# Kernel tuning notes

Hardware: AMD Instinct MI355X
Metric: run time of the kernel (lower is better)

Reference implementation:

```python
import jax, jax.numpy as jnp
import numpy as np

EPS = 1e-5


def reference(hidden_states, mu_x, W_x1, W_x2, x_bias, W_r, W_k, W_v, W_g,
              A_w, B_w, b_w, bonus, gn_weight, gn_bias, W_o):
    B, T, D = hidden_states.shape
    Hh = bonus.shape[0]
    x = hidden_states
    # token shift: delta = shifted(x) - x, shifted pads one zero row at t=0
    shifted = jnp.pad(x, ((0, 0), (1, 0), (0, 0)))[:, :T]
    delta = shifted - x
    # x_proj: LerpLinear(D -> 5*lr) -> tanh -> einsum with second weight viewed [D,5,lr]
    lr = W_x1.shape[0] // 5
    z = jnp.tanh((x + delta * mu_x) @ W_x1.T).reshape(B, T, 5, lr)
    mus = jnp.einsum('blnr,dnr->blnd', z, W_x2.reshape(D, 5, lr)) + x_bias  # [B,T,5,D]
    r_mu, w_mu, k_mu, v_mu, g_mu = (mus[:, :, i] for i in range(5))
    # DDLerpLinear projections: linear(x + delta * mu)
    r = (x + delta * r_mu) @ W_r.T                                 # [B,T,KD]
    w = jnp.tanh((x + delta * w_mu) @ A_w.T) @ B_w.T + b_w          # LoRA w/ tanh
    k = (x + delta * k_mu) @ W_k.T
    v = (x + delta * v_mu) @ W_v.T                                 # [B,T,VD]
    g = (x + delta * g_mu) @ W_g.T
    K = W_r.shape[0] // Hh
    V = W_v.shape[0] // Hh
    r = r.reshape(B, T, Hh, K)
    k = k.reshape(B, T, Hh, K)
    w = -jnp.exp(w.reshape(B, T, Hh, K))  # log-decay, in (-inf, 0)
    v = v.reshape(B, T, Hh, V)
    u = bonus                              # [Hh, K]

    def step(S, inp):
        q_t, k_t, v_t, w_t = inp           # [B,Hh,K],[B,Hh,K],[B,Hh,V],[B,Hh,K]
        kv = k_t[..., :, None] * v_t[..., None, :]                  # [B,Hh,K,V]
        o_t = jnp.einsum('bhk,bhkv->bhv', q_t, S + u[None, :, :, None] * kv)
        S = jnp.exp(w_t)[..., None] * S + kv
        return S, o_t

    S0 = jnp.zeros((B, Hh, K, V), dtype=x.dtype)
    xs = (jnp.swapaxes(r, 0, 1), jnp.swapaxes(k, 0, 1),
          jnp.swapaxes(v, 0, 1), jnp.swapaxes(w, 0, 1))
    _, o = jax.lax.scan(step, S0, xs)       # o: [T,B,Hh,V]
    o = jnp.swapaxes(o, 0, 1)               # [B,T,Hh,V]
    # GroupNorm(num_heads, value_dim): normalize each head's V channels per token
    mean = o.mean(-1, keepdims=True)
    var = o.var(-1, keepdims=True)
    o = (o - mean) / jnp.sqrt(var + EPS)
    o = o.reshape(B, T, Hh * V) * gn_weight + gn_bias
    o = o * jax.nn.silu(g)                  # swish gate
    return o @ W_o.T


def setup_inputs() -> dict:
    key = jax.random.key(0)
    ks = jax.random.split(key, 16)
    B, T, D = 8, 2048, 1024
    Hh, KD, VD, LR, GLR = 4, 512, 1024, 32, 64
    s = 0.02
    w = lambda k, shape: jax.random.normal(k, shape, jnp.float32) * s
    return {
        'hidden_states': jax.random.normal(ks[0], (B, T, D), jnp.float32),
        'mu_x': w(ks[1], (D,)),
        'W_x1': w(ks[2], (5 * LR, D)),
        'W_x2': w(ks[3], (D, 5 * LR)),
        'x_bias': jnp.zeros((5, D), jnp.float32),
        'W_r': w(ks[4], (KD, D)),
        'W_k': w(ks[5], (KD, D)),
        'W_v': w(ks[6], (VD, D)),
        'W_g': w(ks[7], (VD, D)),
        'A_w': w(ks[8], (GLR, D)),
        'B_w': w(ks[9], (KD, GLR)),
        'b_w': jnp.zeros((KD,), jnp.float32),
        'bonus': w(ks[10], (Hh, KD // Hh)),
        'gn_weight': jnp.ones((VD,), jnp.float32),
        'gn_bias': jnp.zeros((VD,), jnp.float32),
        'W_o': w(ks[11], (D, VD)),
    }
```

## Files before the change

### kernel.cpp

```cpp
#include <hip/hip_runtime.h>
#include <hip/hip_bf16.h>
#include <hip/hip_fp16.h>
#include <cstdint>


typedef _Float16 half8 __attribute__((ext_vector_type(8)));
typedef float f32x4 __attribute__((ext_vector_type(4)));
typedef unsigned short ushort8 __attribute__((ext_vector_type(8)));

#define CL 512
#define NP (CL / 2)

__device__ __forceinline__ float hbits2f(unsigned short us) {
    __half h; *reinterpret_cast<unsigned short*>(&h) = us; return __half2float(h);
}
__device__ __forceinline__ unsigned short f2h(float f) {
    __half h = __float2half(f);
    return *reinterpret_cast<unsigned short*>(&h);
}
__device__ __forceinline__ float2 up2(unsigned int u) {
    return make_float2(hbits2f((unsigned short)(u & 0xFFFF)),
                       hbits2f((unsigned short)(u >> 16)));
}

__global__ void cast16(const float* __restrict__ src, __half* __restrict__ dst, int n4)
{
    const int i = blockIdx.x * blockDim.x + threadIdx.x;
    if (i >= n4) return;
    const float4 f = *(const float4*)(src + (size_t)i * 4);
    ushort4 u;
    u.x = f2h(f.x); u.y = f2h(f.y); u.z = f2h(f.z); u.w = f2h(f.w);
    *(ushort4*)(dst + (size_t)i * 4) = u;
}

__global__ void k_xw_h(const float* __restrict__ X, const float* __restrict__ mu,
                       __half* __restrict__ XW, int M, int T)
{
    const size_t i4 = (size_t)blockIdx.x * blockDim.x + threadIdx.x;
    if (i4 >= (size_t)M * 256) return;
    const size_t idx = i4 * 4;
    const int m = (int)(idx >> 10);
    const int d = (int)(idx & 1023);
    const int t = m & (T - 1);
    const float4 xv = *(const float4*)(X + idx);
    const float4 m4 = *(const float4*)(mu + d);
    float4 xp = make_float4(0.f, 0.f, 0.f, 0.f);
    if (t > 0) xp = *(const float4*)(X + idx - 1024);
    ushort4 o;
    o.x = f2h(xv.x + (xp.x - xv.x) * m4.x);
    o.y = f2h(xv.y + (xp.y - xv.y) * m4.y);
    o.z = f2h(xv.z + (xp.z - xv.z) * m4.z);
    o.w = f2h(xv.w + (xp.w - xv.w) * m4.w);
    *(ushort4*)(XW + idx) = o;
}

#define TS 40

__global__ __launch_bounds__(256) void gemm16(
    const __half* __restrict__ A, int lda,
    const __half* __restrict__ B, int ldb,
    void* __restrict__ Cv, int ldc,
    int M, int N, int K,
    const float* __restrict__ bias, int epi,
    const float* __restrict__ X, int T)
{
    __shared__ __align__(16) _Float16 As[128 * TS];
    __shared__ __align__(16) _Float16 Bs[128 * TS];

    const int tid = threadIdx.x;

    const int nwg = gridDim.x * gridDim.y;
    int p = blockIdx.y * gridDim.x + blockIdx.x;
    if (!(nwg & 7)) p = (p & 7) * (nwg >> 3) + (p >> 3);
    const int bx = p % gridDim.x, by = p / gridDim.x;

    const int m0 = by * 128;
    const int n0 = bx * 128;
    const int wave = tid >> 6, lane = tid & 63;
    const int wm = wave >> 1, wn = wave & 1;
    const int lr = lane & 15, lk = lane >> 4;

    const int srow = tid >> 1;
    const int sseg = (tid & 1) * 16;

    f32x4 acc[4][4] = {};

    for (int k0 = 0; k0 < K; k0 += 32) {
        const __half* ap = A + (size_t)(m0 + srow) * lda + k0 + sseg;
        ushort8 a0 = *(const ushort8*)ap;
        ushort8 a1 = *(const ushort8*)(ap + 8);
        ushort8 b0 = {0,0,0,0,0,0,0,0}, b1 = {0,0,0,0,0,0,0,0};
        if (n0 + srow < N) {
            const __half* bp = B + (size_t)(n0 + srow) * ldb + k0 + sseg;
            b0 = *(const ushort8*)bp;
            b1 = *(const ushort8*)(bp + 8);
        }
        __syncthreads();
        *(ushort8*)&As[srow * TS + sseg + 0] = a0;
        *(ushort8*)&As[srow * TS + sseg + 8] = a1;
        *(ushort8*)&Bs[srow * TS + sseg + 0] = b0;
        *(ushort8*)&Bs[srow * TS + sseg + 8] = b1;
        __syncthreads();

        half8 af[4], bf[4];
#pragma unroll
        for (int f = 0; f < 4; f++) {
            af[f] = *(const half8*)&As[(wm * 64 + f * 16 + lr) * TS + lk * 8];
            bf[f] = *(const half8*)&Bs[(wn * 64 + f * 16 + lr) * TS + lk * 8];
        }
#pragma unroll
        for (int fm = 0; fm < 4; fm++)
#pragma unroll
            for (int fn = 0; fn < 4; fn++)
                acc[fm][fn] = __builtin_amdgcn_mfma_f32_16x16x32_f16(
                    af[fm], bf[fn], acc[fm][fn], 0, 0, 0);
    }

#pragma unroll
    for (int fm = 0; fm < 4; fm++) {
#pragma unroll
        for (int fn = 0; fn < 4; fn++) {
#pragma unroll
            for (int j = 0; j < 4; j++) {
                const int gm = m0 + wm * 64 + fm * 16 + lk * 4 + j;
                const int gn = n0 + wn * 64 + fn * 16 + lr;
                if (gn >= N) continue;
                float a = acc[fm][fn][j];
                if (epi == 1) {
                    a = tanhf(a);
                    ((__half*)Cv)[(size_t)gm * ldc + gn] = __float2half(a);
                } else if (epi == 2) {
                    a += bias[gn];
                    const float xv = X[(size_t)gm * 1024 + gn];
                    float xp = 0.f;
                    if (gm & (T - 1)) xp = X[(size_t)(gm - 1) * 1024 + gn];
                    ((__half*)Cv)[(size_t)gm * ldc + gn] =
                        __float2half(xv + (xp - xv) * a);
                } else if (epi == 3) {
                    a += bias[gn];
                    ((__half*)Cv)[(size_t)gm * ldc + gn] = __float2half(a);
                } else if (epi == 4) {
                    ((float*)Cv)[(size_t)gm * ldc + gn] = a;
                } else {
                    ((__half*)Cv)[(size_t)gm * ldc + gn] = __float2half(a);
                }
            }
        }
    }
}

__global__ __launch_bounds__(256) void k_prep(
    const __half* __restrict__ R, const __half* __restrict__ Kk,
    const __half* __restrict__ W, const float* __restrict__ bonus,
    unsigned* __restrict__ Eu, float* __restrict__ RU, int T)
{
    const int tok = blockIdx.x;
    const int b = tok >> 11, t = tok & 2047;
    const int h = threadIdx.x >> 6, lane = threadIdx.x & 63;
    const size_t base = (size_t)tok * 512 + h * 128 + 2 * lane;
    const unsigned rr = *(const unsigned*)(R + base);
    const unsigned kk = *(const unsigned*)(Kk + base);
    const unsigned ww = *(const unsigned*)(W + base);
    const float2 rf = up2(rr), kf = up2(kk), wf = up2(ww);
    const float d0 = __expf(-__expf(wf.x));
    const float d1 = __expf(-__expf(wf.y));
    const float2 uf = *(const float2*)(bonus + h * 128 + 2 * lane);
    float ru = rf.x * uf.x * kf.x + rf.y * uf.y * kf.y;
#pragma unroll
    for (int off = 1; off < 64; off <<= 1) ru += __shfl_xor(ru, off);
    const int bh = b * 4 + h;
    unsigned* ep = Eu + (size_t)(bh * T + t) * 192;
    uint2 rkw;
    rkw.x = (rr & 0xFFFFu) | (kk << 16);
    rkw.y = (rr >> 16) | (kk & 0xFFFF0000u);
    *(uint2*)(ep + 2 * lane) = rkw;
    ep[128 + lane] = (unsigned)f2h(d0) | ((unsigned)f2h(d1) << 16);
    if (lane == 0) RU[(size_t)bh * T + t] = ru;
}

template<bool PART>
__global__ __launch_bounds__(256) void rwkv_coop(
    const uint4* __restrict__ E, const __half* __restrict__ V,
    const float* __restrict__ RU, const float* __restrict__ Cin,
    float* __restrict__ Cout, float* __restrict__ Abuf,
    __half* __restrict__ O, int T)
{
    __shared__ uint4 sE[4][96];
    __shared__ uint4 sV[4][16];
    __shared__ float sRU[4][2];

    const int p = blockIdx.x;
    int bh, c, vq;
    if (PART) {
        const int l = (p & 7) * 48 + (p >> 3);
        bh = l / 12; const int rem = l - bh * 12; c = rem >> 2; vq = rem & 3;
    } else {
        const int l = (p & 7) * 64 + (p >> 3);
        bh = l >> 4; c = (l >> 2) & 3; vq = l & 3;
    }
    const int b = bh >> 2, h = bh & 3;
    const int tid = threadIdx.x;
    const int w = tid >> 6, lane = tid & 63;
    const int kg = tid & 15, vg = tid >> 4;
    const int t0 = c * CL;

    const uint4* Eg = E + (size_t)(bh * T + t0) * 48;
    const uint4* Vgp = (const uint4*)(V + ((size_t)b * T + t0) * 1024 + h * 256 + vq * 64);
    const float* RUp = RU + (size_t)bh * T + t0;
    __half* Op = O + ((size_t)b * T + t0) * 1024 + h * 256 + vq * 64 + vg * 4;

    float S[32];
    float Aacc[8];
    if (!PART && c) {
        const float* Sp = Cin + ((size_t)(c - 1) * 32 + bh) * 32768 + vq * 64 + vg * 4;
#pragma unroll
        for (int kk = 0; kk < 8; kk++) {
            const float4 s4 = *(const float4*)(Sp + (size_t)(kg * 8 + kk) * 256);
            S[kk * 4 + 0] = s4.x; S[kk * 4 + 1] = s4.y;
            S[kk * 4 + 2] = s4.z; S[kk * 4 + 3] = s4.w;
        }
    } else {
#pragma unroll
        for (int j = 0; j < 32; j++) S[j] = 0.f;
    }
#pragma unroll
    for (int j = 0; j < 8; j++) Aacc[j] = 1.f;

    const int i0 = (kg * 2) ^ ((kg * 2) >> 3);
    const int i1 = (kg * 2 + 1) ^ ((kg * 2 + 1) >> 3);

#define ISSUE(BE, BV, BR, PP)                                                 \
    if (w < 2 && (PP) < NP) {                                                 \
        const int tt = (PP) * 2 + w;                                          \
        if (lane < 48)      BE = Eg[(size_t)tt * 48 + lane];                  \
        else if (lane < 56) BV = Vgp[(size_t)tt * 128 + (lane - 48)];         \
        if (lane == 56)     BR = RUp[tt];                                     \
    }

#define STAGE(BE, BV, BR, SLOT)                                               \
    if (w < 2) {                                                              \
        if (lane < 32)      sE[SLOT][w * 48 + (lane ^ (lane >> 3))] = BE;     \
        else if (lane < 48) sE[SLOT][w * 48 + lane] = BE;                     \
        else if (lane < 56) sV[SLOT][w * 8 + (lane - 48)] = BV;               \
        if (lane == 56)     sRU[SLOT][w] = BR;                                \
    }

#define BAR() do {                                                            \
        asm volatile("s_waitcnt lgkmcnt(0)" ::: "memory");                    \
        __builtin_amdgcn_s_barrier();                                         \
        __builtin_amdgcn_sched_barrier(0);                                    \
    } while (0)

#define COMPUTE(SLOT, SUB, TT)                                                \
    {                                                                         \
        const uint4 rka = sE[SLOT][(SUB) * 48 + i0];                          \
        const uint4 rkb = sE[SLOT][(SUB) * 48 + i1];                          \
        const uint4 dq  = sE[SLOT][(SUB) * 48 + 32 + kg];                     \
        const uint2 vw  = *(const uint2*)((const unsigned*)&sV[SLOT][(SUB) * 8] + vg * 2); \
        const unsigned rw_[8] = {rka.x, rka.y, rka.z, rka.w,                  \
                                 rkb.x, rkb.y, rkb.z, rkb.w};                 \
        const unsigned dw_[4] = {dq.x, dq.y, dq.z, dq.w};                     \
        float r_[8], k_[8], d_[8], vv_[4];                                    \
        _Pragma("unroll") for (int j = 0; j < 8; j++) {                       \
            const float2 rk = up2(rw_[j]); r_[j] = rk.x; k_[j] = rk.y;        \
        }                                                                     \
        _Pragma("unroll") for (int j = 0; j < 4; j++) {                       \
            const float2 dd = up2(dw_[j]); d_[2 * j] = dd.x; d_[2 * j + 1] = dd.y; \
        }                                                                     \
        { const float2 va = up2(vw.x), vb = up2(vw.y);                        \
          vv_[0] = va.x; vv_[1] = va.y; vv_[2] = vb.x; vv_[3] = vb.y; }       \
        float osum[4] = {0.f, 0.f, 0.f, 0.f};                                 \
        _Pragma("unroll") for (int kk = 0; kk < 8; kk++) {                    \
            _Pragma("unroll") for (int vi = 0; vi < 4; vi++) {                \
                osum[vi] = fmaf(r_[kk], S[kk * 4 + vi], osum[vi]);            \
                S[kk * 4 + vi] = fmaf(d_[kk], S[kk * 4 + vi], k_[kk] * vv_[vi]); \
            }                                                                 \
            if (PART) Aacc[kk] *= d_[kk];                                     \
        }                                                                     \
        if (!PART) {                                                          \
            _Pragma("unroll") for (int vi = 0; vi < 4; vi++) {                \
                osum[vi] += __shfl_xor(osum[vi], 1);                          \
                osum[vi] += __shfl_xor(osum[vi], 2);                          \
                osum[vi] += __shfl_xor(osum[vi], 4);                          \
                osum[vi] += __shfl_xor(osum[vi], 8);                          \
            }                                                                 \
            if (kg == 0) {                                                    \
                const float ru_ = sRU[SLOT][SUB];                             \
                ushort4 ou;                                                   \
                ou.x = f2h(osum[0] + ru_ * vv_[0]);                           \
                ou.y = f2h(osum[1] + ru_ * vv_[1]);                           \
                ou.z = f2h(osum[2] + ru_ * vv_[2]);                           \
                ou.w = f2h(osum[3] + ru_ * vv_[3]);                           \
                *(ushort4*)(Op + (size_t)(TT) * 1024) = ou;                   \
            }                                                                 \
        }                                                                     \
    }

#define COMPUTE2(SLOT, PP)  COMPUTE(SLOT, 0, (PP) * 2) COMPUTE(SLOT, 1, (PP) * 2 + 1)

    uint4 e0 = {}, e1 = {}, e2 = {}, e3 = {};
    uint4 v0 = {}, v1 = {}, v2 = {}, v3 = {};
    float r0 = 0.f, r1 = 0.f, r2 = 0.f, r3 = 0.f;

    ISSUE(e0, v0, r0, 0)
    ISSUE(e1, v1, r1, 1)
    ISSUE(e2, v2, r2, 2)
    ISSUE(e3, v3, r3, 3)
    STAGE(e0, v0, r0, 0)
    BAR();

    for (int ps = 0; ps < NP; ps += 4) {
        STAGE(e1, v1, r1, 1)
        ISSUE(e0, v0, r0, ps + 4)
        COMPUTE2(0, ps)
        BAR();
        STAGE(e2, v2, r2, 2)
        ISSUE(e1, v1, r1, ps + 5)
        COMPUTE2(1, ps + 1)
        BAR();
        STAGE(e3, v3, r3, 3)
        ISSUE(e2, v2, r2, ps + 6)
        COMPUTE2(2, ps + 2)
        BAR();
        if (ps + 4 < NP) STAGE(e0, v0, r0, 0)
        ISSUE(e3, v3, r3, ps + 7)
        COMPUTE2(3, ps + 3)
        BAR();
    }

    if (PART) {
        float* Cw = Cout + ((size_t)c * 32 + bh) * 32768 + vq * 64 + vg * 4;
#pragma unroll
        for (int kk = 0; kk < 8; kk++) {
            float4 s4;
            s4.x = S[kk * 4 + 0]; s4.y = S[kk * 4 + 1];
            s4.z = S[kk * 4 + 2]; s4.w = S[kk * 4 + 3];
            *(float4*)(Cw + (size_t)(kg * 8 + kk) * 256) = s4;
        }
        if (vg == 0) {
            float* Aw = Abuf + ((size_t)c * 32 + bh) * 128 + kg * 8;
#pragma unroll
            for (int kk = 0; kk < 8; kk++) Aw[kk] = Aacc[kk];
        }
    }
#undef ISSUE
#undef STAGE
#undef BAR
#undef COMPUTE
#undef COMPUTE2
}

__global__ __launch_bounds__(256) void rwkv_comb(
    float* __restrict__ C, const float* __restrict__ A)
{
    const int gid = blockIdx.x * 256 + threadIdx.x;
    const int bh = gid >> 15;
    const int elem = gid & 32767;
    const int k = elem >> 8;
    float s = C[(size_t)bh * 32768 + elem];
    s = A[(size_t)(32 + bh) * 128 + k] * s +
        C[((size_t)32 + bh) * 32768 + elem];
    C[((size_t)32 + bh) * 32768 + elem] = s;
    s = A[(size_t)(64 + bh) * 128 + k] * s +
        C[((size_t)64 + bh) * 32768 + elem];
    C[((size_t)64 + bh) * 32768 + elem] = s;
}

__global__ __launch_bounds__(256) void gn_gate(
    const __half* __restrict__ Obuf, const __half* __restrict__ G,
    const float* __restrict__ gnw, const float* __restrict__ gnb,
    __half* __restrict__ Y)
{
    const int token = blockIdx.x;
    const int wave = threadIdx.x >> 6, lane = threadIdx.x & 63;
    const size_t base = (size_t)token * 1024 + wave * 256 + lane * 4;
    const ushort4 xu = *(const ushort4*)(Obuf + base);
    const float x0 = hbits2f(xu.x), x1 = hbits2f(xu.y),
                x2 = hbits2f(xu.z), x3 = hbits2f(xu.w);
    float sum = x0 + x1 + x2 + x3;
    float ssq = x0 * x0 + x1 * x1 + x2 * x2 + x3 * x3;
#pragma unroll
    for (int off = 32; off >= 1; off >>= 1) {
        sum += __shfl_xor(sum, off);
        ssq += __shfl_xor(ssq, off);
    }
    const float mean = sum * (1.f / 256.f);
    const float var = ssq * (1.f / 256.f) - mean * mean;
    const float rstd = rsqrtf(var + 1e-5f);
    const int c0 = wave * 256 + lane * 4;
    const float4 w4 = *(const float4*)(gnw + c0);
    const float4 b4 = *(const float4*)(gnb + c0);
    const ushort4 gu = *(const ushort4*)(G + base);
    const float g0 = hbits2f(gu.x), g1 = hbits2f(gu.y),
                g2 = hbits2f(gu.z), g3 = hbits2f(gu.w);
    ushort4 y;
    y.x = f2h(((x0 - mean) * rstd * w4.x + b4.x) * (g0 / (1.f + __expf(-g0))));
    y.y = f2h(((x1 - mean) * rstd * w4.y + b4.y) * (g1 / (1.f + __expf(-g1))));
    y.z = f2h(((x2 - mean) * rstd * w4.z + b4.z) * (g2 / (1.f + __expf(-g2))));
    y.w = f2h(((x3 - mean) * rstd * w4.w + b4.w) * (g3 / (1.f + __expf(-g3))));
    *(ushort4*)(Y + base) = y;
}

extern "C" void kernel_launch(void* const* d_in, const int* in_sizes, int n_in,
                              void* d_out, int out_size, void* d_ws, size_t ws_size,
                              hipStream_t stream)
{
    (void)in_sizes; (void)n_in; (void)out_size; (void)ws_size;
    const float* x      = (const float*)d_in[0];
    const float* mu_x   = (const float*)d_in[1];
    const float* W_x1   = (const float*)d_in[2];
    const float* W_x2   = (const float*)d_in[3];
    const float* x_bias = (const float*)d_in[4];
    const float* W_r    = (const float*)d_in[5];
    const float* W_k    = (const float*)d_in[6];
    const float* W_v    = (const float*)d_in[7];
    const float* W_g    = (const float*)d_in[8];
    const float* A_w    = (const float*)d_in[9];
    const float* B_w    = (const float*)d_in[10];
    const float* b_w    = (const float*)d_in[11];
    const float* bonus  = (const float*)d_in[12];
    const float* gnw    = (const float*)d_in[13];
    const float* gnb    = (const float*)d_in[14];
    const float* W_o    = (const float*)d_in[15];

    const int B = 8, T = 2048, M = B * T;

    __half* xwh  = (__half*)d_out;
    __half* inbh = xwh + (size_t)M * 1024;

    __half* z   = (__half*)d_ws;
    __half* w1  = z   + (size_t)M * 160;
    __half* rs  = w1  + (size_t)M * 64;
    __half* ks  = rs  + (size_t)M * 512;
    __half* wsm = ks  + (size_t)M * 512;
    __half* vs  = wsm + (size_t)M * 512;
    __half* gs  = vs  + (size_t)M * 1024;
    float*  ru  = (float*)(gs + (size_t)M * 1024);
    __half* wgt = (__half*)(ru + (size_t)32 * T);
    __half* oh  = rs;
    __half* yb  = wsm;
    float*  Cbuf = (float*)wsm;
    float*  Abuf = (float*)z;

    __half* W_x1h = wgt;
    __half* W_x2h = W_x1h + 163840;
    __half* W_rh  = W_x2h + 163840;
    __half* W_kh  = W_rh + 524288;
    __half* W_vh  = W_kh + 524288;
    __half* W_gh  = W_vh + 1048576;
    __half* A_wh  = W_gh + 1048576;
    __half* B_wh  = A_wh + 65536;
    __half* W_oh  = B_wh + 32768;

    const dim3 blk(256);
    auto cgrid = [](int n) { return dim3((n / 4 + 255) / 256); };
    cast16<<<cgrid(163840), blk, 0, stream>>>(W_x1, W_x1h, 163840 / 4);
    cast16<<<cgrid(163840), blk, 0, stream>>>(W_x2, W_x2h, 163840 / 4);
    cast16<<<cgrid(524288), blk, 0, stream>>>(W_r, W_rh, 524288 / 4);
    cast16<<<cgrid(524288), blk, 0, stream>>>(W_k, W_kh, 524288 / 4);
    cast16<<<cgrid(1048576), blk, 0, stream>>>(W_v, W_vh, 1048576 / 4);
    cast16<<<cgrid(1048576), blk, 0, stream>>>(W_g, W_gh, 1048576 / 4);
    cast16<<<cgrid(65536), blk, 0, stream>>>(A_w, A_wh, 65536 / 4);
    cast16<<<cgrid(32768), blk, 0, stream>>>(B_w, B_wh, 32768 / 4);
    cast16<<<cgrid(1048576), blk, 0, stream>>>(W_o, W_oh, 1048576 / 4);

    k_xw_h<<<(M * 256 + 255) / 256, blk, 0, stream>>>(x, mu_x, xwh, M, T);

    auto ggrid = [&](int N) { return dim3((N + 127) / 128, M / 128); };

    gemm16<<<ggrid(160), blk, 0, stream>>>(xwh, 1024, W_x1h, 1024, z, 160,
                                           M, 160, 1024, nullptr, 1, nullptr, T);

    for (int n = 0; n < 5; ++n) {
        gemm16<<<ggrid(1024), blk, 0, stream>>>(z + n * 32, 160, W_x2h + n * 32, 160,
                                                inbh, 1024, M, 1024, 32,
                                                x_bias + n * 1024, 2, x, T);
        if (n == 1) {
            gemm16<<<ggrid(64), blk, 0, stream>>>(inbh, 1024, A_wh, 1024, w1, 64,
                                                  M, 64, 1024, nullptr, 1, nullptr, T);
            gemm16<<<ggrid(512), blk, 0, stream>>>(w1, 64, B_wh, 64, wsm, 512,
                                                   M, 512, 64, b_w, 3, nullptr, T);
        } else {
            __half* Cp = (n == 0) ? rs : (n == 2) ? ks : (n == 3) ? vs : gs;
            const __half* Wp = (n == 0) ? W_rh : (n == 2) ? W_kh : (n == 3) ? W_vh : W_gh;
            const int N = (n == 0 || n == 2) ? 512 : 1024;
            gemm16<<<ggrid(N), blk, 0, stream>>>(inbh, 1024, Wp, 1024, Cp, N,
                                                 M, N, 1024, nullptr, 0, nullptr, T);
        }
    }

    k_prep<<<dim3(M), blk, 0, stream>>>(rs, ks, wsm, bonus,
                                        (unsigned*)d_out, ru, T);

    rwkv_coop<true><<<dim3(384), blk, 0, stream>>>(
        (const uint4*)d_out, vs, ru, Cbuf, Cbuf, Abuf, oh, T);
    rwkv_comb<<<dim3(4096), blk, 0, stream>>>(Cbuf, Abuf);
    rwkv_coop<false><<<dim3(512), blk, 0, stream>>>(
        (const uint4*)d_out, vs, ru, Cbuf, Cbuf, Abuf, oh, T);

    gn_gate<<<dim3(M), blk, 0, stream>>>(oh, gs, gnw, gnb, yb);

    gemm16<<<ggrid(1024), blk, 0, stream>>>(yb, 1024, W_oh, 1024, d_out, 1024,
                                            M, 1024, 1024, nullptr, 4, nullptr, T);
}
```

Before: 1.222 ms.

## Load GEMM tiles directly to LDS, halve scan chunk length, store carry states in fp16

```diff
diff --git a/kernel.cpp b/kernel.cpp
--- a/kernel.cpp
+++ b/kernel.cpp
@@ -6,10 +6,10 @@
 
 typedef _Float16 half8 __attribute__((ext_vector_type(8)));
 typedef float f32x4 __attribute__((ext_vector_type(4)));
-typedef unsigned short ushort8 __attribute__((ext_vector_type(8)));
-
-#define CL 512
+
+#define CL 256
 #define NP (CL / 2)
+#define NC 8
 
 __device__ __forceinline__ float hbits2f(unsigned short us) {
     __half h; *reinterpret_cast<unsigned short*>(&h) = us; return __half2float(h);
@@ -21,6 +21,11 @@
 __device__ __forceinline__ float2 up2(unsigned int u) {
     return make_float2(hbits2f((unsigned short)(u & 0xFFFF)),
                        hbits2f((unsigned short)(u >> 16)));
+}
+__device__ __forceinline__ void gload_lds16(const void* g, void* l) {
+    __builtin_amdgcn_global_load_lds(
+        (const __attribute__((address_space(1))) unsigned*)g,
+        (__attribute__((address_space(3))) unsigned*)l, 16, 0, 0);
 }
 
 __global__ void cast16(const float* __restrict__ src, __half* __restrict__ dst, int n4)
@@ -54,8 +59,6 @@
     *(ushort4*)(XW + idx) = o;
 }
 
-#define TS 40
-
 __global__ __launch_bounds__(256) void gemm16(
     const __half* __restrict__ A, int lda,
     const __half* __restrict__ B, int ldb,
@@ -64,8 +67,8 @@
     const float* __restrict__ bias, int epi,
     const float* __restrict__ X, int T)
 {
-    __shared__ __align__(16) _Float16 As[128 * TS];
-    __shared__ __align__(16) _Float16 Bs[128 * TS];
+    __shared__ __align__(16) _Float16 As[128 * 32];
+    __shared__ __align__(16) _Float16 Bs[128 * 32];
 
     const int tid = threadIdx.x;
 
@@ -80,33 +83,33 @@
     const int wm = wave >> 1, wn = wave & 1;
     const int lr = lane & 15, lk = lane >> 4;
 
-    const int srow = tid >> 1;
-    const int sseg = (tid & 1) * 16;
+    const int srow = tid >> 2;
+    const int scol = (tid & 3) * 8;
+    const int arow0 = m0 + srow, arow1 = m0 + 64 + srow;
+    int brow0 = n0 + srow;      if (brow0 >= N) brow0 = N - 1;
+    int brow1 = n0 + 64 + srow; if (brow1 >= N) brow1 = N - 1;
+    char* dA = (char*)As + tid * 16;
+    char* dB = (char*)Bs + tid * 16;
 
     f32x4 acc[4][4] = {};
 
     for (int k0 = 0; k0 < K; k0 += 32) {
-        const __half* ap = A + (size_t)(m0 + srow) * lda + k0 + sseg;
-        ushort8 a0 = *(const ushort8*)ap;
-        ushort8 a1 = *(const ushort8*)(ap + 8);
-        ushort8 b0 = {0,0,0,0,0,0,0,0}, b1 = {0,0,0,0,0,0,0,0};
-        if (n0 + srow < N) {
-            const __half* bp = B + (size_t)(n0 + srow) * ldb + k0 + sseg;
-            b0 = *(const ushort8*)bp;
-            b1 = *(const ushort8*)(bp + 8);
-        }
+        const __half* gA0 = A + (size_t)arow0 * lda + k0 + scol;
+        const __half* gA1 = A + (size_t)arow1 * lda + k0 + scol;
+        const __half* gB0 = B + (size_t)brow0 * ldb + k0 + scol;
+        const __half* gB1 = B + (size_t)brow1 * ldb + k0 + scol;
         __syncthreads();
-        *(ushort8*)&As[srow * TS + sseg + 0] = a0;
-        *(ushort8*)&As[srow * TS + sseg + 8] = a1;
-        *(ushort8*)&Bs[srow * TS + sseg + 0] = b0;
-        *(ushort8*)&Bs[srow * TS + sseg + 8] = b1;
+        gload_lds16(gA0, dA);
+        gload_lds16(gA1, dA + 4096);
+        gload_lds16(gB0, dB);
+        gload_lds16(gB1, dB + 4096);
         __syncthreads();
 
         half8 af[4], bf[4];
 #pragma unroll
         for (int f = 0; f < 4; f++) {
-            af[f] = *(const half8*)&As[(wm * 64 + f * 16 + lr) * TS + lk * 8];
-            bf[f] = *(const half8*)&Bs[(wn * 64 + f * 16 + lr) * TS + lk * 8];
+            af[f] = *(const half8*)&As[(wm * 64 + f * 16 + lr) * 32 + lk * 8];
+            bf[f] = *(const half8*)&Bs[(wn * 64 + f * 16 + lr) * 32 + lk * 8];
         }
 #pragma unroll
         for (int fm = 0; fm < 4; fm++)
@@ -181,8 +184,8 @@
 template<bool PART>
 __global__ __launch_bounds__(256) void rwkv_coop(
     const uint4* __restrict__ E, const __half* __restrict__ V,
-    const float* __restrict__ RU, const float* __restrict__ Cin,
-    float* __restrict__ Cout, float* __restrict__ Abuf,
+    const float* __restrict__ RU, const __half* __restrict__ Cin,
+    __half* __restrict__ Cout, float* __restrict__ Abuf,
     __half* __restrict__ O, int T)
 {
     __shared__ uint4 sE[4][96];
@@ -192,11 +195,11 @@
     const int p = blockIdx.x;
     int bh, c, vq;
     if (PART) {
-        const int l = (p & 7) * 48 + (p >> 3);
-        bh = l / 12; const int rem = l - bh * 12; c = rem >> 2; vq = rem & 3;
+        const int l = (p & 7) * 112 + (p >> 3);
+        bh = l / 28; const int rem = l - bh * 28; c = rem >> 2; vq = rem & 3;
     } else {
-        const int l = (p & 7) * 64 + (p >> 3);
-        bh = l >> 4; c = (l >> 2) & 3; vq = l & 3;
+        const int l = (p & 7) * 128 + (p >> 3);
+        bh = l >> 5; c = (l >> 2) & 7; vq = l & 3;
     }
     const int b = bh >> 2, h = bh & 3;
     const int tid = threadIdx.x;
@@ -212,12 +215,12 @@
     float S[32];
     float Aacc[8];
     if (!PART && c) {
-        const float* Sp = Cin + ((size_t)(c - 1) * 32 + bh) * 32768 + vq * 64 + vg * 4;
+        const __half* Sp = Cin + ((size_t)(c - 1) * 32 + bh) * 32768 + vq * 64 + vg * 4;
 #pragma unroll
         for (int kk = 0; kk < 8; kk++) {
-            const float4 s4 = *(const float4*)(Sp + (size_t)(kg * 8 + kk) * 256);
-            S[kk * 4 + 0] = s4.x; S[kk * 4 + 1] = s4.y;
-            S[kk * 4 + 2] = s4.z; S[kk * 4 + 3] = s4.w;
+            const ushort4 s4 = *(const ushort4*)(Sp + (size_t)(kg * 8 + kk) * 256);
+            S[kk * 4 + 0] = hbits2f(s4.x); S[kk * 4 + 1] = hbits2f(s4.y);
+            S[kk * 4 + 2] = hbits2f(s4.z); S[kk * 4 + 3] = hbits2f(s4.w);
         }
     } else {
 #pragma unroll
@@ -329,13 +332,13 @@
     }
 
     if (PART) {
-        float* Cw = Cout + ((size_t)c * 32 + bh) * 32768 + vq * 64 + vg * 4;
+        __half* Cw = Cout + ((size_t)c * 32 + bh) * 32768 + vq * 64 + vg * 4;
 #pragma unroll
         for (int kk = 0; kk < 8; kk++) {
-            float4 s4;
-            s4.x = S[kk * 4 + 0]; s4.y = S[kk * 4 + 1];
-            s4.z = S[kk * 4 + 2]; s4.w = S[kk * 4 + 3];
-            *(float4*)(Cw + (size_t)(kg * 8 + kk) * 256) = s4;
+            ushort4 s4;
+            s4.x = f2h(S[kk * 4 + 0]); s4.y = f2h(S[kk * 4 + 1]);
+            s4.z = f2h(S[kk * 4 + 2]); s4.w = f2h(S[kk * 4 + 3]);
+            *(ushort4*)(Cw + (size_t)(kg * 8 + kk) * 256) = s4;
         }
         if (vg == 0) {
             float* Aw = Abuf + ((size_t)c * 32 + bh) * 128 + kg * 8;
@@ -351,19 +354,20 @@
 }
 
 __global__ __launch_bounds__(256) void rwkv_comb(
-    float* __restrict__ C, const float* __restrict__ A)
+    __half* __restrict__ C, const float* __restrict__ A)
 {
     const int gid = blockIdx.x * 256 + threadIdx.x;
     const int bh = gid >> 15;
     const int elem = gid & 32767;
     const int k = elem >> 8;
-    float s = C[(size_t)bh * 32768 + elem];
-    s = A[(size_t)(32 + bh) * 128 + k] * s +
-        C[((size_t)32 + bh) * 32768 + elem];
-    C[((size_t)32 + bh) * 32768 + elem] = s;
-    s = A[(size_t)(64 + bh) * 128 + k] * s +
-        C[((size_t)64 + bh) * 32768 + elem];
-    C[((size_t)64 + bh) * 32768 + elem] = s;
+    float s = hbits2f(*(const unsigned short*)(C + (size_t)bh * 32768 + elem));
+#pragma unroll
+    for (int c = 1; c < NC - 1; ++c) {
+        const float a = A[(size_t)(c * 32 + bh) * 128 + k];
+        __half* cp = C + ((size_t)c * 32 + bh) * 32768 + elem;
+        s = a * s + hbits2f(*(const unsigned short*)cp);
+        *(unsigned short*)cp = f2h(s);
+    }
 }
 
 __global__ __launch_bounds__(256) void gn_gate(
@@ -439,7 +443,7 @@
     __half* wgt = (__half*)(ru + (size_t)32 * T);
     __half* oh  = rs;
     __half* yb  = wsm;
-    float*  Cbuf = (float*)wsm;
+    __half* Cbuf = wsm;
     float*  Abuf = (float*)z;
 
     __half* W_x1h = wgt;
@@ -492,10 +496,10 @@
     k_prep<<<dim3(M), blk, 0, stream>>>(rs, ks, wsm, bonus,
                                         (unsigned*)d_out, ru, T);
 
-    rwkv_coop<true><<<dim3(384), blk, 0, stream>>>(
+    rwkv_coop<true><<<dim3(896), blk, 0, stream>>>(
         (const uint4*)d_out, vs, ru, Cbuf, Cbuf, Abuf, oh, T);
     rwkv_comb<<<dim3(4096), blk, 0, stream>>>(Cbuf, Abuf);
-    rwkv_coop<false><<<dim3(512), blk, 0, stream>>>(
+    rwkv_coop<false><<<dim3(1024), blk, 0, stream>>>(
         (const uint4*)d_out, vs, ru, Cbuf, Cbuf, Abuf, oh, T);
 
     gn_gate<<<dim3(M), blk, 0, stream>>>(oh, gs, gnw, gnb, yb);
```

New measurement: 1.205 ms. About the same (-1.4%).
